# Optimization experiments

Measured on AMD Instinct MI355X. Metric: run time of the kernel, lower is better.

The kernel has to match this reference:

```python
import jax, jax.numpy as jnp
import numpy as np

N_CIRC, N_MI, N_DIS = 40000, 15000, 8000
F_IN, HID, HEADS, OUT = 128, 64, 4, 64
E_CM, E_MD, E_CD = 400000, 300000, 300000
SIZES = (N_CIRC, N_MI, N_DIS)
# relation r: (src_type, dst_type) indices into [circ, mi, dis]
RELS = [(0, 1), (1, 2), (0, 2), (1, 0), (2, 1), (2, 0)]
EDGE_N = [E_CM, E_MD, E_CD, E_CM, E_MD, E_CD]


def _edges(k, n_src, n_dst, n_e):
    k1, k2 = jax.random.split(k)
    src = jax.random.randint(k1, (n_e,), 0, n_src, dtype=jnp.int32)
    dst = jax.random.randint(k2, (n_e,), 0, n_dst, dtype=jnp.int32)
    return jnp.stack([src, dst])


def setup_inputs() -> dict:
    key = jax.random.key(0)
    ks = jax.random.split(key, 20)
    x_circ = jax.random.normal(ks[0], (N_CIRC, F_IN), jnp.float32)
    x_mi = jax.random.normal(ks[1], (N_MI, F_IN), jnp.float32)
    x_dis = jax.random.normal(ks[2], (N_DIS, F_IN), jnp.float32)
    ed = [_edges(ks[3 + r], SIZES[RELS[r][0]], SIZES[RELS[r][1]], EDGE_N[r]) for r in range(6)]
    s1 = 1.0 / np.sqrt(F_IN)
    s2 = 1.0 / np.sqrt(HID * HEADS)
    W1 = jax.random.normal(ks[10], (6, F_IN, HEADS * HID), jnp.float32) * s1
    as1 = jax.random.normal(ks[11], (6, HEADS, HID), jnp.float32) * s2
    ad1 = jax.random.normal(ks[12], (6, HEADS, HID), jnp.float32) * s2
    b1 = jnp.zeros((6, HEADS * HID), jnp.float32)
    W2 = jax.random.normal(ks[13], (6, HEADS * HID, OUT), jnp.float32) * s2
    as2 = jax.random.normal(ks[14], (6, 1, OUT), jnp.float32) * s2
    ad2 = jax.random.normal(ks[15], (6, 1, OUT), jnp.float32) * s2
    b2 = jnp.zeros((6, OUT), jnp.float32)
    return {"x_circ": x_circ, "x_mi": x_mi, "x_dis": x_dis,
            "e_cm": ed[0], "e_md": ed[1], "e_cd": ed[2],
            "e_mc": ed[3], "e_dm": ed[4], "e_dc": ed[5],
            "W1": W1, "as1": as1, "ad1": ad1, "b1": b1,
            "W2": W2, "as2": as2, "ad2": ad2, "b2": b2}


def _gat(x_src, x_dst, src, dst, W, a_s, a_d, b, n_dst, concat):
    # PyG GATConv (shared lin for src/dst), add_self_loops=False, eval mode.
    H, C = a_s.shape
    h_src = (x_src @ W).reshape(-1, H, C)   # [Ns,H,C]
    h_dst = (x_dst @ W).reshape(-1, H, C)   # [Nd,H,C]
    al_s = jnp.einsum('nhc,hc->nh', h_src, a_s)
    al_d = jnp.einsum('nhc,hc->nh', h_dst, a_d)
    e = jax.nn.leaky_relu(al_s[src] + al_d[dst], 0.2)           # [E,H]
    m = jax.ops.segment_max(e, dst, num_segments=n_dst)         # [Nd,H]
    m = jnp.where(jnp.isfinite(m), m, 0.0)
    ex = jnp.exp(e - m[dst])
    den = jax.ops.segment_sum(ex, dst, num_segments=n_dst)
    alpha = ex / (den[dst] + 1e-16)                             # scatter-softmax
    msg = h_src[src] * alpha[:, :, None]                        # [E,H,C]
    out = jax.ops.segment_sum(msg.reshape(-1, H * C), dst, num_segments=n_dst)
    out = out.reshape(n_dst, H, C)
    return (out.reshape(n_dst, H * C) if concat else out.mean(axis=1)) + b


def _hetero(xs, edges, W, a_s, a_d, b, concat):
    acc = [[] for _ in xs]
    for r, (s, d) in enumerate(RELS):
        o = _gat(xs[s], xs[d], edges[r][0], edges[r][1], W[r], a_s[r], a_d[r], b[r], SIZES[d], concat)
        acc[d].append(o)
    return [jnp.mean(jnp.stack(lst), axis=0) for lst in acc]  # aggr='mean'


def reference(x_circ, x_mi, x_dis, e_cm, e_md, e_cd, e_mc, e_dm, e_dc,
              W1, as1, ad1, b1, W2, as2, ad2, b2):
    xs = [x_circ, x_mi, x_dis]
    edges = [e_cm, e_md, e_cd, e_mc, e_dm, e_dc]
    h = _hetero(xs, edges, W1, as1, ad1, b1, concat=True)
    h = [jax.nn.elu(v) for v in h]  # dropout is identity in eval
    h = _hetero(h, edges, W2, as2, ad2, b2, concat=False)
    out = [v / jnp.maximum(jnp.linalg.norm(v, axis=1, keepdims=True), 1e-12) for v in h]
    return tuple(out)
```

## Files before the change

### kernel.cpp

```cpp
#include <hip/hip_runtime.h>
#include <hip/hip_bf16.h>
#include <math.h>

#define NCIRC 40000
#define NMI   15000
#define NDIS  8000
#define NTOT  (NCIRC + NMI + NDIS)
#define OFFSTR 40064

typedef __hip_bfloat16 bf16;
typedef __attribute__((ext_vector_type(8))) short short8;
typedef __attribute__((ext_vector_type(4))) float f32x4;
typedef __attribute__((ext_vector_type(8))) unsigned short us8v;

static __device__ __forceinline__ float us2f(unsigned short u){ return __uint_as_float(((unsigned)u) << 16); }
static __device__ __forceinline__ unsigned short f2bu(float v){
    bf16 t = __float2bfloat16(v);
    return *reinterpret_cast<unsigned short*>(&t);
}
static __device__ __forceinline__ float ldx(const void* p, size_t i, int f32){
    return f32 ? ((const float*)p)[i] : __bfloat162float(((const bf16*)p)[i]);
}
static inline unsigned cdiv(long long a, long long b){ return (unsigned)((a + b - 1) / b); }

struct CsrArgs {
    const int* src[6]; const int* dst[6];
    int ecnt[6]; int eoff[6]; int nd[6];
};
struct ScanArgs { int start[6]; int nch[6]; int nd[6]; };
struct Al1Args { const void* x[3]; const float* wa[3][4]; float* out[3][4]; int nt[3]; };
struct Al2Args { const unsigned short* x[3]; const float* wa[3][4]; float* out[3][4]; int nt[3]; };
struct GemmArgs { const void* A[6]; unsigned long long bOff[6]; unsigned long long cOff[6];
                  int M[6]; int nblk[6]; };
struct GatArgs {
    const unsigned short* srcs[3][2]; const int* off[3][2];
    const float* als[3][2]; const float* ald[3][2];
    const unsigned short* hs[3][2];
};
struct P1Args {
    CsrArgs ca;
    const void *W1, *as1, *ad1, *W2, *as2, *ad2, *b1, *b2;
    float *WA1S, *WA1D, *WA2S, *WA2D, *BIAS1, *BIAS2;
    bf16 *W1T, *W2T;
    int *CNT;
    int eTw1, eTw2, eWa1, eWa2, eBias;
    int nbCnt[6];
};
struct P2Args {
    CsrArgs ca;
    const int* OFF; int* POS; unsigned short* SRCS;
    GemmArgs g1;
    Al1Args a1;
    int eFill, eGemm;
    int nbCnt[6];
    int nbAl[3];
};
struct P3Args {
    Al2Args a2;
    GemmArgs g2;
    int eAl2;
    int nbAl[3];
};
struct P2ArgsFix { P2Args p; const bf16* W1T; bf16* HS1; };
struct P3ArgsFix { P3Args p; const bf16* W2T; bf16* HS2; };

__global__ void init_k(const unsigned short* __restrict__ u, int* __restrict__ flag,
                       int* __restrict__ zbase, int zcount){
    if (blockIdx.x == 0){
        __shared__ int sbad;
        if (threadIdx.x == 0) sbad = 0;
        __syncthreads();
        int bad = 0;
        for (int i = threadIdx.x; i < 4096; i += 256){
            int e = (u[i] >> 7) & 0xFF;
            if (e >= 0x90) bad = 1;
        }
        if (bad) atomicOr(&sbad, 1);
        __syncthreads();
        if (threadIdx.x == 0) *flag = sbad;
    } else {
        for (int i = (blockIdx.x - 1)*256 + threadIdx.x; i < zcount; i += 63*256)
            zbase[i] = 0;
    }
}

static __device__ __forceinline__ void tw_body(const void* W, int f32, bf16* WT,
                                               int Kd, int Nd, int nrel, int blk){
    long long idx = (long long)blk * 256 + threadIdx.x;
    long long tot = (long long)nrel * Kd * Nd;
    if (idx >= tot) return;
    int per = Kd * Nd;
    int r = (int)(idx / per);
    int rem = (int)(idx % per);
    int n = rem / Kd, k = rem % Kd;
    float v = ldx(W, (size_t)r*per + (size_t)k*Nd + n, f32);
    WT[idx] = __float2bfloat16(v);
}

static __device__ __forceinline__ void wa1_body(const void* W1, const void* as1, const void* ad1,
                                                int f32, float* wa_s, float* wa_d, int blk){
    int r = blk >> 1;
    int t = (blk & 1)*256 + threadIdx.x;
    int f = t >> 2, h = t & 3;
    size_t wb = (size_t)r*128*256 + (size_t)f*256 + h*64;
    size_t ab = (size_t)r*256 + h*64;
    float ss = 0.f, sd = 0.f;
    for (int c = 0; c < 64; c++){
        float w = ldx(W1, wb + c, f32);
        ss += w * ldx(as1, ab + c, f32);
        sd += w * ldx(ad1, ab + c, f32);
    }
    wa_s[r*512 + t] = ss; wa_d[r*512 + t] = sd;
}

static __device__ __forceinline__ void wa2_body(const void* W2, const void* as2, const void* ad2,
                                                int f32, float* wa_s, float* wa_d, int r){
    int f = threadIdx.x;
    size_t wb = (size_t)r*256*64 + (size_t)f*64;
    float ss = 0.f, sd = 0.f;
    for (int c = 0; c < 64; c++){
        float w = ldx(W2, wb + c, f32);
        ss += w * ldx(as2, (size_t)r*64 + c, f32);
        sd += w * ldx(ad2, (size_t)r*64 + c, f32);
    }
    wa_s[r*256 + f] = ss; wa_d[r*256 + f] = sd;
}

static __device__ __forceinline__ void bias_body(const void* b1, const void* b2, int f32,
                                                 float* BIAS1, float* BIAS2, int t){
    const int relA[3] = {3, 0, 1};
    const int relB[3] = {5, 4, 2};
    int c = threadIdx.x;
    BIAS1[t*256 + c] = 0.5f*(ldx(b1, relA[t]*256 + c, f32) + ldx(b1, relB[t]*256 + c, f32));
    if (c < 64)
        BIAS2[t*64 + c] = 0.5f*(ldx(b2, relA[t]*64 + c, f32) + ldx(b2, relB[t]*64 + c, f32));
}

static __device__ void al1_body(const Al1Args& a, int f32, int t, int blk, float (*swa)[512]){
    int N = a.nt[t];
    for (int i = threadIdx.x; i < 2048; i += 256) swa[i >> 9][i & 511] = a.wa[t][i >> 9][i & 511];
    __syncthreads();
    int n = blk * 256 + threadIdx.x;
    if (n >= N) return;
    float s[4][4] = {};
    if (f32){
        const float* xr = (const float*)a.x[t] + (size_t)n*128;
        for (int f = 0; f < 128; f++){
            float v = xr[f];
            #pragma unroll
            for (int j = 0; j < 4; j++){
                s[j][0] += v*swa[j][f*4+0]; s[j][1] += v*swa[j][f*4+1];
                s[j][2] += v*swa[j][f*4+2]; s[j][3] += v*swa[j][f*4+3];
            }
        }
    } else {
        const unsigned short* xr = (const unsigned short*)a.x[t] + (size_t)n*128;
        for (int f0 = 0; f0 < 128; f0 += 8){
            us8v v8 = *(const us8v*)(xr + f0);
            #pragma unroll
            for (int jj = 0; jj < 8; jj++){
                float v = us2f(v8[jj]); int f = f0 + jj;
                #pragma unroll
                for (int j = 0; j < 4; j++){
                    s[j][0] += v*swa[j][f*4+0]; s[j][1] += v*swa[j][f*4+1];
                    s[j][2] += v*swa[j][f*4+2]; s[j][3] += v*swa[j][f*4+3];
                }
            }
        }
    }
    #pragma unroll
    for (int j = 0; j < 4; j++)
        *(float4*)(a.out[t][j] + (size_t)n*4) = make_float4(s[j][0], s[j][1], s[j][2], s[j][3]);
}

static __device__ void al2_body(const Al2Args& a, int t, int blk, float (*swa)[256]){
    int N = a.nt[t];
    for (int i = threadIdx.x; i < 1024; i += 256) swa[i >> 8][i & 255] = a.wa[t][i >> 8][i & 255];
    __syncthreads();
    int n = blk * 256 + threadIdx.x;
    if (n >= N) return;
    const unsigned short* xr = a.x[t] + (size_t)n*256;
    float s0 = 0.f, s1 = 0.f, s2 = 0.f, s3 = 0.f;
    for (int f0 = 0; f0 < 256; f0 += 8){
        us8v v8 = *(const us8v*)(xr + f0);
        #pragma unroll
        for (int jj = 0; jj < 8; jj++){
            float v = us2f(v8[jj]); int f = f0 + jj;
            s0 += v*swa[0][f]; s1 += v*swa[1][f]; s2 += v*swa[2][f]; s3 += v*swa[3][f];
        }
    }
    a.out[t][0][n] = s0; a.out[t][1][n] = s1; a.out[t][2][n] = s2; a.out[t][3][n] = s3;
}

static __device__ void gemm_body(const GemmArgs& ga, int af32, const bf16* WT,
                                 bf16* Cb, int N, int K, int nIdx, int yTot,
                                 unsigned short (*As)[40], unsigned short (*Bs)[40]){
    int y = yTot, r = 0;
    while (r < 5 && y >= ga.nblk[r]){ y -= ga.nblk[r]; r++; }
    int M = ga.M[r];
    int m0 = y * 64, n0 = nIdx * 64;
    const void* A = ga.A[r];
    const unsigned short* WTu = (const unsigned short*)WT + ga.bOff[r];
    bf16* C = Cb + ga.cOff[r];
    int tid = threadIdx.x;
    int w = tid >> 6, lane = tid & 63;
    int quad = lane >> 4, l16 = lane & 15;
    int srow = tid >> 2, skc = (tid & 3) * 8;
    f32x4 acc[4] = {};
    for (int k0 = 0; k0 < K; k0 += 32){
        {
            int gr = m0 + srow;
            us8v av;
            if (gr < M){
                if (af32){
                    const float* ap = (const float*)A + (size_t)gr*K + k0 + skc;
                    #pragma unroll
                    for (int j = 0; j < 8; j++) av[j] = f2bu(ap[j]);
                } else {
                    av = *(const us8v*)((const unsigned short*)A + (size_t)gr*K + k0 + skc);
                }
            } else {
                #pragma unroll
                for (int j = 0; j < 8; j++) av[j] = 0;
            }
            *(us8v*)&As[srow][skc] = av;
        }
        *(us8v*)&Bs[srow][skc] = *(const us8v*)(WTu + (size_t)(n0 + srow)*K + k0 + skc);
        __syncthreads();
        short8 af = *(const short8*)&As[w*16 + l16][quad*8];
        #pragma unroll
        for (int c = 0; c < 4; c++){
            short8 bfv = *(const short8*)&Bs[c*16 + l16][quad*8];
            acc[c] = __builtin_amdgcn_mfma_f32_16x16x32_bf16(af, bfv, acc[c], 0, 0, 0);
        }
        __syncthreads();
    }
    #pragma unroll
    for (int c = 0; c < 4; c++){
        #pragma unroll
        for (int i = 0; i < 4; i++){
            int m = m0 + w*16 + quad*4 + i;
            if (m < M) C[(size_t)m*N + n0 + c*16 + l16] = __float2bfloat16(acc[c][i]);
        }
    }
}

__global__ void p1_k(P1Args p, const int* __restrict__ flag){
    int bid = blockIdx.x;
    int f32 = *flag;
    if (bid < p.eTw1){
        tw_body(p.W1, f32, p.W1T, 128, 256, 6, bid);
    } else if (bid < p.eTw2){
        tw_body(p.W2, f32, p.W2T, 256, 64, 6, bid - p.eTw1);
    } else if (bid < p.eWa1){
        wa1_body(p.W1, p.as1, p.ad1, f32, p.WA1S, p.WA1D, bid - p.eTw2);
    } else if (bid < p.eWa2){
        wa2_body(p.W2, p.as2, p.ad2, f32, p.WA2S, p.WA2D, bid - p.eWa1);
    } else if (bid < p.eBias){
        bias_body(p.b1, p.b2, f32, p.BIAS1, p.BIAS2, bid - p.eWa2);
    } else {
        int b = bid - p.eBias, r = 0;
        while (r < 5 && b >= p.nbCnt[r]){ b -= p.nbCnt[r]; r++; }
        int e = b*256 + threadIdx.x;
        if (e < p.ca.ecnt[r]) atomicAdd(&p.CNT[r*OFFSTR + p.ca.dst[r][e]], 1);
    }
}

__global__ void scan_a(ScanArgs s, const int* __restrict__ cnt, int* __restrict__ off,
                       int* __restrict__ CHT){
    int b = blockIdx.x, r = 0;
    while (r < 5 && b >= s.start[r+1]) r++;
    int chunk = b - s.start[r];
    int N = s.nd[r];
    int tid = threadIdx.x, lane = tid & 63, wv = tid >> 6;
    __shared__ int wsum[16];
    int i = chunk*1024 + tid;
    int x = (i < N) ? cnt[r*OFFSTR + i] : 0;
    #pragma unroll
    for (int d = 1; d < 64; d <<= 1){
        int y = __shfl_up(x, d, 64);
        if (lane >= d) x += y;
    }
    if (lane == 63) wsum[wv] = x;
    __syncthreads();
    if (tid == 0){
        int acc = 0;
        #pragma unroll
        for (int k = 0; k < 16; k++){ acc += wsum[k]; wsum[k] = acc; }
    }
    __syncthreads();
    int incl = x + ((wv == 0) ? 0 : wsum[wv - 1]);
    if (i < N) off[r*OFFSTR + i + 1] = incl;
    if (tid == 1023) CHT[r*64 + chunk] = incl;
}

__global__ void scan_b(ScanArgs s, int* __restrict__ CHT){
    int r = threadIdx.x;
    if (r < 6){
        int acc = 0;
        for (int c = 0; c < s.nch[r]; c++){
            int v = CHT[r*64 + c];
            CHT[r*64 + c] = acc;
            acc += v;
        }
    }
}

__global__ void scan_c(ScanArgs s, int* __restrict__ off, const int* __restrict__ CHT){
    int b = blockIdx.x, r = 0;
    while (r < 5 && b >= s.start[r+1]) r++;
    int chunk = b - s.start[r];
    int N = s.nd[r];
    int i = chunk*1024 + threadIdx.x;
    int addv = CHT[r*64 + chunk];
    if (i < N) off[r*OFFSTR + i + 1] += addv;
    if (chunk == 0 && threadIdx.x == 0) off[r*OFFSTR] = 0;
}

__global__ void p2_kf(P2ArgsFix q, const int* __restrict__ flag){
    __shared__ __align__(16) char smem[10240];
    P2Args& p = q.p;
    int bid = blockIdx.x;
    if (bid < p.eFill){
        int b = bid, r = 0;
        while (r < 5 && b >= p.nbCnt[r]){ b -= p.nbCnt[r]; r++; }
        int e = b*256 + threadIdx.x;
        if (e < p.ca.ecnt[r]){
            int d = p.ca.dst[r][e];
            int pos = atomicAdd(&p.POS[r*OFFSTR + d], 1);
            p.SRCS[p.ca.eoff[r] + p.OFF[r*OFFSTR + d] + pos] = (unsigned short)p.ca.src[r][e];
        }
    } else if (bid < p.eGemm){
        int id = bid - p.eFill;
        int nIdx = id & 3, yTot = id >> 2;
        unsigned short (*As)[40] = (unsigned short(*)[40])smem;
        unsigned short (*Bs)[40] = (unsigned short(*)[40])(smem + 5120);
        gemm_body(p.g1, *flag, q.W1T, q.HS1, 256, 128, nIdx, yTot, As, Bs);
    } else {
        int b = bid - p.eGemm, t = 0;
        while (t < 2 && b >= p.nbAl[t]){ b -= p.nbAl[t]; t++; }
        al1_body(p.a1, *flag, t, b, (float(*)[512])smem);
    }
}

__global__ void p3_kf(P3ArgsFix q){
    __shared__ __align__(16) char smem[10240];
    P3Args& p = q.p;
    int bid = blockIdx.x;
    if (bid < p.eAl2){
        int b = bid, t = 0;
        while (t < 2 && b >= p.nbAl[t]){ b -= p.nbAl[t]; t++; }
        al2_body(p.a2, t, b, (float(*)[256])smem);
    } else {
        int yTot = bid - p.eAl2;
        unsigned short (*As)[40] = (unsigned short(*)[40])smem;
        unsigned short (*Bs)[40] = (unsigned short(*)[40])(smem + 5120);
        gemm_body(p.g2, 0, q.W2T, q.HS2, 64, 256, 0, yTot, As, Bs);
    }
}

__global__ void gat_l1(GatArgs g, const float* __restrict__ BIAS1,
                       unsigned short* __restrict__ X2B){
    int gw = blockIdx.x * 4 + (threadIdx.x >> 6);
    if (gw >= NTOT) return;
    int t, w;
    if (gw < NCIRC){ t = 0; w = gw; }
    else if (gw < NCIRC + NMI){ t = 1; w = gw - NCIRC; }
    else { t = 2; w = gw - NCIRC - NMI; }
    int lane = threadIdx.x & 63;
    int hw = lane >> 5, l32 = lane & 31;
    int h = l32 >> 3;
    float fT[8] = {0.f,0.f,0.f,0.f,0.f,0.f,0.f,0.f};
    #pragma unroll
    for (int a = 0; a < 2; a++){
        const float* als = g.als[t][a];
        const unsigned short* srcs = g.srcs[t][a];
        const unsigned short* Hu = g.hs[t][a];
        float aldv = g.ald[t][a][(size_t)w*4 + h];
        int beg = g.off[t][a][w], end = g.off[t][a][w+1];
        float fa[8] = {0.f,0.f,0.f,0.f,0.f,0.f,0.f,0.f};
        float den = 0.f;
        int i = beg + hw;
        for (; i + 6 < end; i += 8){
            int s0 = srcs[i], s1 = srcs[i+2], s2 = srcs[i+4], s3 = srcs[i+6];
            us8v v0 = *(const us8v*)(Hu + (size_t)s0*256 + l32*8);
            us8v v1 = *(const us8v*)(Hu + (size_t)s1*256 + l32*8);
            us8v v2 = *(const us8v*)(Hu + (size_t)s2*256 + l32*8);
            us8v v3 = *(const us8v*)(Hu + (size_t)s3*256 + l32*8);
            float x0 = als[(size_t)s0*4 + h] + aldv;
            float x1 = als[(size_t)s1*4 + h] + aldv;
            float x2 = als[(size_t)s2*4 + h] + aldv;
            float x3 = als[(size_t)s3*4 + h] + aldv;
            float e0 = __expf(x0 > 0.f ? x0 : 0.2f*x0);
            float e1 = __expf(x1 > 0.f ? x1 : 0.2f*x1);
            float e2 = __expf(x2 > 0.f ? x2 : 0.2f*x2);
            float e3 = __expf(x3 > 0.f ? x3 : 0.2f*x3);
            den += e0 + e1 + e2 + e3;
            #pragma unroll
            for (int k = 0; k < 8; k++)
                fa[k] += e0*us2f(v0[k]) + e1*us2f(v1[k]) + e2*us2f(v2[k]) + e3*us2f(v3[k]);
        }
        for (; i < end; i += 2){
            int s = srcs[i];
            us8v v = *(const us8v*)(Hu + (size_t)s*256 + l32*8);
            float xv = als[(size_t)s*4 + h] + aldv;
            float e = __expf(xv > 0.f ? xv : 0.2f*xv);
            den += e;
            #pragma unroll
            for (int k = 0; k < 8; k++) fa[k] += e*us2f(v[k]);
        }
        den += __shfl_xor(den, 32, 64);
        float inv = 1.0f / (den + 1e-16f);
        #pragma unroll
        for (int k = 0; k < 8; k++) fT[k] += fa[k]*inv;
    }
    #pragma unroll
    for (int k = 0; k < 8; k++) fT[k] += __shfl_xor(fT[k], 32, 64);
    if (hw == 0){
        const float* bp = BIAS1 + t*256 + l32*8;
        us8v st;
        #pragma unroll
        for (int k = 0; k < 8; k++){
            float v = fT[k]*0.5f + bp[k];
            v = v > 0.f ? v : (__expf(v) - 1.f);
            st[k] = f2bu(v);
        }
        *(us8v*)(X2B + (size_t)gw*256 + l32*8) = st;
    }
}

__global__ void gat_l2(GatArgs g, const float* __restrict__ BIAS2,
                       void* __restrict__ out, const int* __restrict__ flag){
    int gw = blockIdx.x * 4 + (threadIdx.x >> 6);
    if (gw >= NTOT) return;
    int t, w;
    if (gw < NCIRC){ t = 0; w = gw; }
    else if (gw < NCIRC + NMI){ t = 1; w = gw - NCIRC; }
    else { t = 2; w = gw - NCIRC - NMI; }
    int lane = threadIdx.x & 63;
    int qw = lane >> 4, l16 = lane & 15;
    float fT[4] = {0.f,0.f,0.f,0.f};
    #pragma unroll
    for (int a = 0; a < 2; a++){
        const float* als = g.als[t][a];
        const unsigned short* srcs = g.srcs[t][a];
        const unsigned short* Hu = g.hs[t][a];
        float aldv = g.ald[t][a][w];
        int beg = g.off[t][a][w], end = g.off[t][a][w+1];
        float fa[4] = {0.f,0.f,0.f,0.f};
        float den = 0.f;
        int i = beg + qw;
        for (; i + 12 < end; i += 16){
            int s0 = srcs[i], s1 = srcs[i+4], s2 = srcs[i+8], s3 = srcs[i+12];
            ushort4 v0 = *(const ushort4*)(Hu + (size_t)s0*64 + l16*4);
            ushort4 v1 = *(const ushort4*)(Hu + (size_t)s1*64 + l16*4);
            ushort4 v2 = *(const ushort4*)(Hu + (size_t)s2*64 + l16*4);
            ushort4 v3 = *(const ushort4*)(Hu + (size_t)s3*64 + l16*4);
            float x0 = als[s0] + aldv, x1 = als[s1] + aldv;
            float x2 = als[s2] + aldv, x3 = als[s3] + aldv;
            float e0 = __expf(x0 > 0.f ? x0 : 0.2f*x0);
            float e1 = __expf(x1 > 0.f ? x1 : 0.2f*x1);
            float e2 = __expf(x2 > 0.f ? x2 : 0.2f*x2);
            float e3 = __expf(x3 > 0.f ? x3 : 0.2f*x3);
            den += e0 + e1 + e2 + e3;
            fa[0] += e0*us2f(v0.x) + e1*us2f(v1.x) + e2*us2f(v2.x) + e3*us2f(v3.x);
            fa[1] += e0*us2f(v0.y) + e1*us2f(v1.y) + e2*us2f(v2.y) + e3*us2f(v3.y);
            fa[2] += e0*us2f(v0.z) + e1*us2f(v1.z) + e2*us2f(v2.z) + e3*us2f(v3.z);
            fa[3] += e0*us2f(v0.w) + e1*us2f(v1.w) + e2*us2f(v2.w) + e3*us2f(v3.w);
        }
        for (; i < end; i += 4){
            int s = srcs[i];
            ushort4 v = *(const ushort4*)(Hu + (size_t)s*64 + l16*4);
            float xv = als[s] + aldv;
            float e = __expf(xv > 0.f ? xv : 0.2f*xv);
            den += e;
            fa[0] += e*us2f(v.x); fa[1] += e*us2f(v.y);
            fa[2] += e*us2f(v.z); fa[3] += e*us2f(v.w);
        }
        den += __shfl_xor(den, 32, 64);
        den += __shfl_xor(den, 16, 64);
        float inv = 1.0f / (den + 1e-16f);
        #pragma unroll
        for (int k = 0; k < 4; k++) fT[k] += fa[k]*inv;
    }
    #pragma unroll
    for (int k = 0; k < 4; k++){
        fT[k] += __shfl_xor(fT[k], 32, 64);
        fT[k] += __shfl_xor(fT[k], 16, 64);
    }
    const float* bp = BIAS2 + t*64 + l16*4;
    float v0 = fT[0]*0.5f + bp[0];
    float v1 = fT[1]*0.5f + bp[1];
    float v2 = fT[2]*0.5f + bp[2];
    float v3 = fT[3]*0.5f + bp[3];
    float ss = v0*v0 + v1*v1 + v2*v2 + v3*v3;
    #pragma unroll
    for (int mk = 8; mk > 0; mk >>= 1) ss += __shfl_xor(ss, mk, 64);
    float nrm = sqrtf(ss);
    nrm = nrm > 1e-12f ? nrm : 1e-12f;
    float inv_n = 1.0f / nrm;
    if (qw == 0){
        size_t base = (size_t)gw*64 + l16*4;
        if (*flag){
            *(float4*)((float*)out + base) = make_float4(v0*inv_n, v1*inv_n, v2*inv_n, v3*inv_n);
        } else {
            ushort4 st;
            st.x = f2bu(v0*inv_n); st.y = f2bu(v1*inv_n);
            st.z = f2bu(v2*inv_n); st.w = f2bu(v3*inv_n);
            *(ushort4*)((unsigned short*)out + base) = st;
        }
    }
}

extern "C" void kernel_launch(void* const* d_in, const int* in_sizes, int n_in,
                              void* d_out, int out_size, void* d_ws, size_t ws_size,
                              hipStream_t stream){
    const void* x[3] = {d_in[0], d_in[1], d_in[2]};
    const int Nt[3] = {NCIRC, NMI, NDIS};
    const int* ep[6]; int Ecnt[6];
    for (int r = 0; r < 6; r++){ ep[r] = (const int*)d_in[3 + r]; Ecnt[r] = in_sizes[3 + r] / 2; }
    const void* W1  = d_in[9];
    const void* as1 = d_in[10];
    const void* ad1 = d_in[11];
    const void* b1  = d_in[12];
    const void* W2  = d_in[13];
    const void* as2 = d_in[14];
    const void* ad2 = d_in[15];
    const void* b2  = d_in[16];

    const int rs[6] = {0, 1, 0, 1, 2, 2};
    const int rd[6] = {1, 2, 2, 0, 1, 0};
    const int srel[3][2] = {{0, 2}, {1, 3}, {4, 5}};
    const int drel[3][2] = {{3, 5}, {0, 4}, {1, 2}};
    const int accRow[3] = {0, NCIRC, NCIRC + NMI};

    float* ws    = (float*)d_ws;
    int*   FLAG  = (int*)ws;
    float* WA1S  = ws + 16;
    float* WA1D  = WA1S + 6*512;
    float* WA2S  = WA1D + 6*512;
    float* WA2D  = WA2S + 6*256;
    float* BIAS1 = WA2D + 6*256;
    float* BIAS2 = BIAS1 + 768;
    float* ALB   = BIAS2 + 192;
    unsigned short* HS1u = (unsigned short*)(ALB + 1008000);
    unsigned short* HS2u = HS1u + 32256000;
    unsigned short* X2Bu = HS2u + 8064000;
    bf16*  W1T   = (bf16*)(X2Bu + 16128000);
    bf16*  W2T   = W1T + 6*256*128;
    int*   CNT   = (int*)(W2T + 6*64*256);
    int*   POS   = CNT + 6*OFFSTR;
    int*   OFF   = POS + 6*OFFSTR;
    int*   CHT   = OFF + 6*OFFSTR;
    unsigned short* SRCS = (unsigned short*)(CHT + 6*64);

    int eOff[6]; int acc_e = 0;
    for (int r = 0; r < 6; r++){ eOff[r] = acc_e; acc_e += Ecnt[r]; }
    unsigned long long hs1off[6], hs2off[6];
    { unsigned long long o1 = 0, o2 = 0;
      for (int r = 0; r < 6; r++){ hs1off[r] = o1; o1 += (unsigned long long)Nt[rs[r]]*256;
                                   hs2off[r] = o2; o2 += (unsigned long long)Nt[rs[r]]*64; } }
    float *AL1S[6], *AL1D[6], *AL2S[6], *AL2D[6];
    { size_t o = 0;
      for (int r = 0; r < 6; r++){ AL1S[r] = ALB + o; o += (size_t)Nt[rs[r]]*4; }
      for (int r = 0; r < 6; r++){ AL1D[r] = ALB + o; o += (size_t)Nt[rd[r]]*4; }
      size_t o2 = 0;
      for (int r = 0; r < 6; r++){ AL2S[r] = ALB + o2; o2 += (size_t)Nt[rs[r]]; }
      for (int r = 0; r < 6; r++){ AL2D[r] = ALB + o2; o2 += (size_t)Nt[rd[r]]; } }

    CsrArgs ca;
    for (int r = 0; r < 6; r++){
        ca.src[r] = ep[r]; ca.dst[r] = ep[r] + Ecnt[r];
        ca.ecnt[r] = Ecnt[r]; ca.eoff[r] = eOff[r]; ca.nd[r] = Nt[rd[r]];
    }

    init_k<<<64, 256, 0, stream>>>((const unsigned short*)d_in[0], FLAG, CNT, 12*OFFSTR);

    P1Args p1;
    p1.ca = ca;
    p1.W1 = W1; p1.as1 = as1; p1.ad1 = ad1; p1.W2 = W2; p1.as2 = as2; p1.ad2 = ad2;
    p1.b1 = b1; p1.b2 = b2;
    p1.WA1S = WA1S; p1.WA1D = WA1D; p1.WA2S = WA2S; p1.WA2D = WA2D;
    p1.BIAS1 = BIAS1; p1.BIAS2 = BIAS2;
    p1.W1T = W1T; p1.W2T = W2T; p1.CNT = CNT;
    int nTw1 = cdiv(6LL*128*256, 256), nTw2 = cdiv(6LL*256*64, 256);
    p1.eTw1 = nTw1; p1.eTw2 = nTw1 + nTw2;
    p1.eWa1 = p1.eTw2 + 12; p1.eWa2 = p1.eWa1 + 6; p1.eBias = p1.eWa2 + 3;
    int cntBlk = 0;
    for (int r = 0; r < 6; r++){ p1.nbCnt[r] = cdiv(Ecnt[r], 256); cntBlk += p1.nbCnt[r]; }
    p1_k<<<p1.eBias + cntBlk, 256, 0, stream>>>(p1, FLAG);

    ScanArgs sa;
    int scBlk = 0;
    for (int r = 0; r < 6; r++){
        sa.start[r] = scBlk;
        sa.nd[r] = Nt[rd[r]];
        sa.nch[r] = cdiv(Nt[rd[r]], 1024);
        scBlk += sa.nch[r];
    }
    scan_a<<<scBlk, 1024, 0, stream>>>(sa, CNT, OFF, CHT);
    scan_b<<<1, 64, 0, stream>>>(sa, CHT);
    scan_c<<<scBlk, 1024, 0, stream>>>(sa, OFF, CHT);

    P2ArgsFix q2;
    q2.p.ca = ca; q2.p.OFF = OFF; q2.p.POS = POS; q2.p.SRCS = SRCS;
    int totBlk1 = 0;
    for (int r = 0; r < 6; r++){
        q2.p.g1.A[r] = x[rs[r]]; q2.p.g1.bOff[r] = (unsigned long long)r*256*128;
        q2.p.g1.cOff[r] = hs1off[r]; q2.p.g1.M[r] = Nt[rs[r]];
        q2.p.g1.nblk[r] = cdiv(Nt[rs[r]], 64); totBlk1 += q2.p.g1.nblk[r];
        q2.p.nbCnt[r] = p1.nbCnt[r];
    }
    for (int t = 0; t < 3; t++){
        q2.p.a1.x[t] = x[t]; q2.p.a1.nt[t] = Nt[t];
        q2.p.nbAl[t] = cdiv(Nt[t], 256);
        for (int j = 0; j < 2; j++){
            q2.p.a1.wa[t][j]   = WA1S + srel[t][j]*512;  q2.p.a1.out[t][j]   = AL1S[srel[t][j]];
            q2.p.a1.wa[t][j+2] = WA1D + drel[t][j]*512;  q2.p.a1.out[t][j+2] = AL1D[drel[t][j]];
        }
    }
    q2.p.eFill = cntBlk; q2.p.eGemm = cntBlk + 4*totBlk1;
    q2.W1T = W1T; q2.HS1 = (bf16*)HS1u;
    int nAl1 = q2.p.nbAl[0] + q2.p.nbAl[1] + q2.p.nbAl[2];
    p2_kf<<<q2.p.eGemm + nAl1, 256, 0, stream>>>(q2, FLAG);

    GatArgs gl1;
    for (int t = 0; t < 3; t++)
        for (int a = 0; a < 2; a++){
            int r = drel[t][a];
            gl1.srcs[t][a] = SRCS + eOff[r]; gl1.off[t][a] = OFF + r*OFFSTR;
            gl1.als[t][a] = AL1S[r]; gl1.ald[t][a] = AL1D[r];
            gl1.hs[t][a] = HS1u + hs1off[r];
        }
    gat_l1<<<cdiv(NTOT, 4), 256, 0, stream>>>(gl1, BIAS1, X2Bu);

    P3ArgsFix q3;
    int totBlk2 = 0;
    for (int r = 0; r < 6; r++){
        q3.p.g2.A[r] = X2Bu + (size_t)accRow[rs[r]]*256;
        q3.p.g2.bOff[r] = (unsigned long long)r*64*256;
        q3.p.g2.cOff[r] = hs2off[r]; q3.p.g2.M[r] = Nt[rs[r]];
        q3.p.g2.nblk[r] = cdiv(Nt[rs[r]], 64); totBlk2 += q3.p.g2.nblk[r];
    }
    for (int t = 0; t < 3; t++){
        q3.p.a2.x[t] = X2Bu + (size_t)accRow[t]*256; q3.p.a2.nt[t] = Nt[t];
        q3.p.nbAl[t] = cdiv(Nt[t], 256);
        for (int j = 0; j < 2; j++){
            q3.p.a2.wa[t][j]   = WA2S + srel[t][j]*256;  q3.p.a2.out[t][j]   = AL2S[srel[t][j]];
            q3.p.a2.wa[t][j+2] = WA2D + drel[t][j]*256;  q3.p.a2.out[t][j+2] = AL2D[drel[t][j]];
        }
    }
    q3.p.eAl2 = q3.p.nbAl[0] + q3.p.nbAl[1] + q3.p.nbAl[2];
    q3.W2T = W2T; q3.HS2 = (bf16*)HS2u;
    p3_kf<<<q3.p.eAl2 + totBlk2, 256, 0, stream>>>(q3);

    GatArgs gl2;
    for (int t = 0; t < 3; t++)
        for (int a = 0; a < 2; a++){
            int r = drel[t][a];
            gl2.srcs[t][a] = SRCS + eOff[r]; gl2.off[t][a] = OFF + r*OFFSTR;
            gl2.als[t][a] = AL2S[r]; gl2.ald[t][a] = AL2D[r];
            gl2.hs[t][a] = HS2u + hs2off[r];
        }
    gat_l2<<<cdiv(NTOT, 4), 256, 0, stream>>>(gl2, BIAS2, d_out, FLAG);
}
```

Baseline: 607.4 us.

## Record edge slots during counting, drop scan fixup pass, fuse layer-2 attention logits

The counting pass now keeps the atomic return value as each edge's slot within its destination. The CSR fill can then place edges without a second atomic pass or a POS buffer. The scan writes exclusive per-chunk offsets and consumers add the chunk total on the fly, which removes the scan_c kernel. The layer-2 attention logit projection is fused into gat_l1's epilogue, using the fp32 ELU outputs and wave shuffles, so the separate al2 pass that re-read X2B is gone. This adds an extra EPOS buffer of 16-bit slots, which assumes in-degree stays below 65536, and a little extra index arithmetic in the GAT kernels.

Result: faster. 547.3 us (-9.9%).

```diff
diff --git a/kernel.cpp b/kernel.cpp
--- a/kernel.cpp
+++ b/kernel.cpp
@@ -29,40 +29,35 @@
 };
 struct ScanArgs { int start[6]; int nch[6]; int nd[6]; };
 struct Al1Args { const void* x[3]; const float* wa[3][4]; float* out[3][4]; int nt[3]; };
-struct Al2Args { const unsigned short* x[3]; const float* wa[3][4]; float* out[3][4]; int nt[3]; };
 struct GemmArgs { const void* A[6]; unsigned long long bOff[6]; unsigned long long cOff[6];
                   int M[6]; int nblk[6]; };
 struct GatArgs {
     const unsigned short* srcs[3][2]; const int* off[3][2];
+    const int* cnt[3][2]; const int* cht[3][2];
     const float* als[3][2]; const float* ald[3][2];
     const unsigned short* hs[3][2];
+    const float* wa2[3][4];
+    float* al2o[3][4];
 };
 struct P1Args {
     CsrArgs ca;
     const void *W1, *as1, *ad1, *W2, *as2, *ad2, *b1, *b2;
     float *WA1S, *WA1D, *WA2S, *WA2D, *BIAS1, *BIAS2;
     bf16 *W1T, *W2T;
-    int *CNT;
+    int *CNT; unsigned short* EPOS;
     int eTw1, eTw2, eWa1, eWa2, eBias;
     int nbCnt[6];
 };
 struct P2Args {
     CsrArgs ca;
-    const int* OFF; int* POS; unsigned short* SRCS;
+    const int* OFF; const int* CHT; const unsigned short* EPOS; unsigned short* SRCS;
     GemmArgs g1;
     Al1Args a1;
     int eFill, eGemm;
     int nbCnt[6];
     int nbAl[3];
 };
-struct P3Args {
-    Al2Args a2;
-    GemmArgs g2;
-    int eAl2;
-    int nbAl[3];
-};
 struct P2ArgsFix { P2Args p; const bf16* W1T; bf16* HS1; };
-struct P3ArgsFix { P3Args p; const bf16* W2T; bf16* HS2; };
 
 __global__ void init_k(const unsigned short* __restrict__ u, int* __restrict__ flag,
                        int* __restrict__ zbase, int zcount){
@@ -171,25 +166,6 @@
     #pragma unroll
     for (int j = 0; j < 4; j++)
         *(float4*)(a.out[t][j] + (size_t)n*4) = make_float4(s[j][0], s[j][1], s[j][2], s[j][3]);
-}
-
-static __device__ void al2_body(const Al2Args& a, int t, int blk, float (*swa)[256]){
-    int N = a.nt[t];
-    for (int i = threadIdx.x; i < 1024; i += 256) swa[i >> 8][i & 255] = a.wa[t][i >> 8][i & 255];
-    __syncthreads();
-    int n = blk * 256 + threadIdx.x;
-    if (n >= N) return;
-    const unsigned short* xr = a.x[t] + (size_t)n*256;
-    float s0 = 0.f, s1 = 0.f, s2 = 0.f, s3 = 0.f;
-    for (int f0 = 0; f0 < 256; f0 += 8){
-        us8v v8 = *(const us8v*)(xr + f0);
-        #pragma unroll
-        for (int jj = 0; jj < 8; jj++){
-            float v = us2f(v8[jj]); int f = f0 + jj;
-            s0 += v*swa[0][f]; s1 += v*swa[1][f]; s2 += v*swa[2][f]; s3 += v*swa[3][f];
-        }
-    }
-    a.out[t][0][n] = s0; a.out[t][1][n] = s1; a.out[t][2][n] = s2; a.out[t][3][n] = s3;
 }
 
 static __device__ void gemm_body(const GemmArgs& ga, int af32, const bf16* WT,
@@ -262,7 +238,11 @@
         int b = bid - p.eBias, r = 0;
         while (r < 5 && b >= p.nbCnt[r]){ b -= p.nbCnt[r]; r++; }
         int e = b*256 + threadIdx.x;
-        if (e < p.ca.ecnt[r]) atomicAdd(&p.CNT[r*OFFSTR + p.ca.dst[r][e]], 1);
+        if (e < p.ca.ecnt[r]){
+            int d = p.ca.dst[r][e];
+            int pos = atomicAdd(&p.CNT[r*OFFSTR + d], 1);
+            p.EPOS[p.ca.eoff[r] + e] = (unsigned short)pos;
+        }
     }
 }
 
@@ -275,7 +255,8 @@
     int tid = threadIdx.x, lane = tid & 63, wv = tid >> 6;
     __shared__ int wsum[16];
     int i = chunk*1024 + tid;
-    int x = (i < N) ? cnt[r*OFFSTR + i] : 0;
+    int v = (i < N) ? cnt[r*OFFSTR + i] : 0;
+    int x = v;
     #pragma unroll
     for (int d = 1; d < 64; d <<= 1){
         int y = __shfl_up(x, d, 64);
@@ -290,7 +271,7 @@
     }
     __syncthreads();
     int incl = x + ((wv == 0) ? 0 : wsum[wv - 1]);
-    if (i < N) off[r*OFFSTR + i + 1] = incl;
+    if (i < N) off[r*OFFSTR + i] = incl - v;
     if (tid == 1023) CHT[r*64 + chunk] = incl;
 }
 
@@ -304,17 +285,6 @@
             acc += v;
         }
     }
-}
-
-__global__ void scan_c(ScanArgs s, int* __restrict__ off, const int* __restrict__ CHT){
-    int b = blockIdx.x, r = 0;
-    while (r < 5 && b >= s.start[r+1]) r++;
-    int chunk = b - s.start[r];
-    int N = s.nd[r];
-    int i = chunk*1024 + threadIdx.x;
-    int addv = CHT[r*64 + chunk];
-    if (i < N) off[r*OFFSTR + i + 1] += addv;
-    if (chunk == 0 && threadIdx.x == 0) off[r*OFFSTR] = 0;
 }
 
 __global__ void p2_kf(P2ArgsFix q, const int* __restrict__ flag){
@@ -327,8 +297,9 @@
         int e = b*256 + threadIdx.x;
         if (e < p.ca.ecnt[r]){
             int d = p.ca.dst[r][e];
-            int pos = atomicAdd(&p.POS[r*OFFSTR + d], 1);
-            p.SRCS[p.ca.eoff[r] + p.OFF[r*OFFSTR + d] + pos] = (unsigned short)p.ca.src[r][e];
+            int beg = p.OFF[r*OFFSTR + d] + p.CHT[r*64 + (d >> 10)];
+            p.SRCS[p.ca.eoff[r] + beg + p.EPOS[p.ca.eoff[r] + e]] =
+                (unsigned short)p.ca.src[r][e];
         }
     } else if (bid < p.eGemm){
         int id = bid - p.eFill;
@@ -343,20 +314,11 @@
     }
 }
 
-__global__ void p3_kf(P3ArgsFix q){
+__global__ void gemm2_k(GemmArgs g2, const bf16* __restrict__ W2T, bf16* __restrict__ HS2){
     __shared__ __align__(16) char smem[10240];
-    P3Args& p = q.p;
-    int bid = blockIdx.x;
-    if (bid < p.eAl2){
-        int b = bid, t = 0;
-        while (t < 2 && b >= p.nbAl[t]){ b -= p.nbAl[t]; t++; }
-        al2_body(p.a2, t, b, (float(*)[256])smem);
-    } else {
-        int yTot = bid - p.eAl2;
-        unsigned short (*As)[40] = (unsigned short(*)[40])smem;
-        unsigned short (*Bs)[40] = (unsigned short(*)[40])(smem + 5120);
-        gemm_body(p.g2, 0, q.W2T, q.HS2, 64, 256, 0, yTot, As, Bs);
-    }
+    unsigned short (*As)[40] = (unsigned short(*)[40])smem;
+    unsigned short (*Bs)[40] = (unsigned short(*)[40])(smem + 5120);
+    gemm_body(g2, 0, W2T, HS2, 64, 256, 0, blockIdx.x, As, Bs);
 }
 
 __global__ void gat_l1(GatArgs g, const float* __restrict__ BIAS1,
@@ -377,7 +339,8 @@
         const unsigned short* srcs = g.srcs[t][a];
         const unsigned short* Hu = g.hs[t][a];
         float aldv = g.ald[t][a][(size_t)w*4 + h];
-        int beg = g.off[t][a][w], end = g.off[t][a][w+1];
+        int beg = g.off[t][a][w] + g.cht[t][a][w >> 10];
+        int end = beg + g.cnt[t][a][w];
         float fa[8] = {0.f,0.f,0.f,0.f,0.f,0.f,0.f,0.f};
         float den = 0.f;
         int i = beg + hw;
@@ -418,14 +381,34 @@
     for (int k = 0; k < 8; k++) fT[k] += __shfl_xor(fT[k], 32, 64);
     if (hw == 0){
         const float* bp = BIAS1 + t*256 + l32*8;
+        float v[8];
         us8v st;
         #pragma unroll
         for (int k = 0; k < 8; k++){
-            float v = fT[k]*0.5f + bp[k];
-            v = v > 0.f ? v : (__expf(v) - 1.f);
-            st[k] = f2bu(v);
+            float vv = fT[k]*0.5f + bp[k];
+            vv = vv > 0.f ? vv : (__expf(vv) - 1.f);
+            v[k] = vv;
+            st[k] = f2bu(vv);
         }
         *(us8v*)(X2B + (size_t)gw*256 + l32*8) = st;
+        float s0 = 0.f, s1 = 0.f, s2 = 0.f, s3 = 0.f;
+        const float* w0 = g.wa2[t][0] + l32*8;
+        const float* w1 = g.wa2[t][1] + l32*8;
+        const float* w2 = g.wa2[t][2] + l32*8;
+        const float* w3 = g.wa2[t][3] + l32*8;
+        #pragma unroll
+        for (int k = 0; k < 8; k++){
+            s0 += v[k]*w0[k]; s1 += v[k]*w1[k]; s2 += v[k]*w2[k]; s3 += v[k]*w3[k];
+        }
+        #pragma unroll
+        for (int mk = 16; mk > 0; mk >>= 1){
+            s0 += __shfl_xor(s0, mk, 64); s1 += __shfl_xor(s1, mk, 64);
+            s2 += __shfl_xor(s2, mk, 64); s3 += __shfl_xor(s3, mk, 64);
+        }
+        if (l32 == 0){
+            g.al2o[t][0][w] = s0; g.al2o[t][1][w] = s1;
+            g.al2o[t][2][w] = s2; g.al2o[t][3][w] = s3;
+        }
     }
 }
 
@@ -446,7 +429,8 @@
         const unsigned short* srcs = g.srcs[t][a];
         const unsigned short* Hu = g.hs[t][a];
         float aldv = g.ald[t][a][w];
-        int beg = g.off[t][a][w], end = g.off[t][a][w+1];
+        int beg = g.off[t][a][w] + g.cht[t][a][w >> 10];
+        int end = beg + g.cnt[t][a][w];
         float fa[4] = {0.f,0.f,0.f,0.f};
         float den = 0.f;
         int i = beg + qw;
@@ -543,16 +527,16 @@
     float* BIAS1 = WA2D + 6*256;
     float* BIAS2 = BIAS1 + 768;
     float* ALB   = BIAS2 + 192;
-    unsigned short* HS1u = (unsigned short*)(ALB + 1008000);
+    unsigned short* HS1u = (unsigned short*)(ALB + 1260000);
     unsigned short* HS2u = HS1u + 32256000;
     unsigned short* X2Bu = HS2u + 8064000;
     bf16*  W1T   = (bf16*)(X2Bu + 16128000);
     bf16*  W2T   = W1T + 6*256*128;
     int*   CNT   = (int*)(W2T + 6*64*256);
-    int*   POS   = CNT + 6*OFFSTR;
-    int*   OFF   = POS + 6*OFFSTR;
+    int*   OFF   = CNT + 6*OFFSTR;
     int*   CHT   = OFF + 6*OFFSTR;
-    unsigned short* SRCS = (unsigned short*)(CHT + 6*64);
+    unsigned short* EPOS = (unsigned short*)(CHT + 6*64);
+    unsigned short* SRCS = EPOS + 2000000;
 
     int eOff[6]; int acc_e = 0;
     for (int r = 0; r < 6; r++){ eOff[r] = acc_e; acc_e += Ecnt[r]; }
@@ -564,7 +548,7 @@
     { size_t o = 0;
       for (int r = 0; r < 6; r++){ AL1S[r] = ALB + o; o += (size_t)Nt[rs[r]]*4; }
       for (int r = 0; r < 6; r++){ AL1D[r] = ALB + o; o += (size_t)Nt[rd[r]]*4; }
-      size_t o2 = 0;
+      size_t o2 = 1008000;
       for (int r = 0; r < 6; r++){ AL2S[r] = ALB + o2; o2 += (size_t)Nt[rs[r]]; }
       for (int r = 0; r < 6; r++){ AL2D[r] = ALB + o2; o2 += (size_t)Nt[rd[r]]; } }
 
@@ -574,7 +558,7 @@
         ca.ecnt[r] = Ecnt[r]; ca.eoff[r] = eOff[r]; ca.nd[r] = Nt[rd[r]];
     }
 
-    init_k<<<64, 256, 0, stream>>>((const unsigned short*)d_in[0], FLAG, CNT, 12*OFFSTR);
+    init_k<<<64, 256, 0, stream>>>((const unsigned short*)d_in[0], FLAG, CNT, 6*OFFSTR);
 
     P1Args p1;
     p1.ca = ca;
@@ -582,7 +566,7 @@
     p1.b1 = b1; p1.b2 = b2;
     p1.WA1S = WA1S; p1.WA1D = WA1D; p1.WA2S = WA2S; p1.WA2D = WA2D;
     p1.BIAS1 = BIAS1; p1.BIAS2 = BIAS2;
-    p1.W1T = W1T; p1.W2T = W2T; p1.CNT = CNT;
+    p1.W1T = W1T; p1.W2T = W2T; p1.CNT = CNT; p1.EPOS = EPOS;
     int nTw1 = cdiv(6LL*128*256, 256), nTw2 = cdiv(6LL*256*64, 256);
     p1.eTw1 = nTw1; p1.eTw2 = nTw1 + nTw2;
     p1.eWa1 = p1.eTw2 + 12; p1.eWa2 = p1.eWa1 + 6; p1.eBias = p1.eWa2 + 3;
@@ -600,10 +584,9 @@
     }
     scan_a<<<scBlk, 1024, 0, stream>>>(sa, CNT, OFF, CHT);
     scan_b<<<1, 64, 0, stream>>>(sa, CHT);
-    scan_c<<<scBlk, 1024, 0, stream>>>(sa, OFF, CHT);
 
     P2ArgsFix q2;
-    q2.p.ca = ca; q2.p.OFF = OFF; q2.p.POS = POS; q2.p.SRCS = SRCS;
+    q2.p.ca = ca; q2.p.OFF = OFF; q2.p.CHT = CHT; q2.p.EPOS = EPOS; q2.p.SRCS = SRCS;
     int totBlk1 = 0;
     for (int r = 0; r < 6; r++){
         q2.p.g1.A[r] = x[rs[r]]; q2.p.g1.bOff[r] = (unsigned long long)r*256*128;
@@ -625,40 +608,37 @@
     p2_kf<<<q2.p.eGemm + nAl1, 256, 0, stream>>>(q2, FLAG);
 
     GatArgs gl1;
-    for (int t = 0; t < 3; t++)
+    for (int t = 0; t < 3; t++){
         for (int a = 0; a < 2; a++){
             int r = drel[t][a];
             gl1.srcs[t][a] = SRCS + eOff[r]; gl1.off[t][a] = OFF + r*OFFSTR;
+            gl1.cnt[t][a] = CNT + r*OFFSTR; gl1.cht[t][a] = CHT + r*64;
             gl1.als[t][a] = AL1S[r]; gl1.ald[t][a] = AL1D[r];
             gl1.hs[t][a] = HS1u + hs1off[r];
         }
+        for (int j = 0; j < 2; j++){
+            gl1.wa2[t][j]   = WA2S + srel[t][j]*256;  gl1.al2o[t][j]   = AL2S[srel[t][j]];
+            gl1.wa2[t][j+2] = WA2D + drel[t][j]*256;  gl1.al2o[t][j+2] = AL2D[drel[t][j]];
+        }
+    }
     gat_l1<<<cdiv(NTOT, 4), 256, 0, stream>>>(gl1, BIAS1, X2Bu);
 
-    P3ArgsFix q3;
+    GemmArgs g2;
     int totBlk2 = 0;
     for (int r = 0; r < 6; r++){
-        q3.p.g2.A[r] = X2Bu + (size_t)accRow[rs[r]]*256;
-        q3.p.g2.bOff[r] = (unsigned long long)r*64*256;
-        q3.p.g2.cOff[r] = hs2off[r]; q3.p.g2.M[r] = Nt[rs[r]];
-        q3.p.g2.nblk[r] = cdiv(Nt[rs[r]], 64); totBlk2 += q3.p.g2.nblk[r];
-    }
-    for (int t = 0; t < 3; t++){
-        q3.p.a2.x[t] = X2Bu + (size_t)accRow[t]*256; q3.p.a2.nt[t] = Nt[t];
-        q3.p.nbAl[t] = cdiv(Nt[t], 256);
-        for (int j = 0; j < 2; j++){
-            q3.p.a2.wa[t][j]   = WA2S + srel[t][j]*256;  q3.p.a2.out[t][j]   = AL2S[srel[t][j]];
-            q3.p.a2.wa[t][j+2] = WA2D + drel[t][j]*256;  q3.p.a2.out[t][j+2] = AL2D[drel[t][j]];
-        }
-    }
-    q3.p.eAl2 = q3.p.nbAl[0] + q3.p.nbAl[1] + q3.p.nbAl[2];
-    q3.W2T = W2T; q3.HS2 = (bf16*)HS2u;
-    p3_kf<<<q3.p.eAl2 + totBlk2, 256, 0, stream>>>(q3);
+        g2.A[r] = X2Bu + (size_t)accRow[rs[r]]*256;
+        g2.bOff[r] = (unsigned long long)r*64*256;
+        g2.cOff[r] = hs2off[r]; g2.M[r] = Nt[rs[r]];
+        g2.nblk[r] = cdiv(Nt[rs[r]], 64); totBlk2 += g2.nblk[r];
+    }
+    gemm2_k<<<totBlk2, 256, 0, stream>>>(g2, W2T, (bf16*)HS2u);
 
     GatArgs gl2;
     for (int t = 0; t < 3; t++)
         for (int a = 0; a < 2; a++){
             int r = drel[t][a];
             gl2.srcs[t][a] = SRCS + eOff[r]; gl2.off[t][a] = OFF + r*OFFSTR;
+            gl2.cnt[t][a] = CNT + r*OFFSTR; gl2.cht[t][a] = CHT + r*64;
             gl2.als[t][a] = AL2S[r]; gl2.ald[t][a] = AL2D[r];
             gl2.hs[t][a] = HS2u + hs2off[r];
         }
```
